# Performance work log

Measured on AMD Instinct MI355X. Metric: run time of the kernel, lower is better.

Reference implementation:

```python
import jax, jax.numpy as jnp
import numpy as np

N = 65536
H = 1024
E = 3  # experts: SwishGLU, GEGLU, ReGLU


def setup_inputs() -> dict:
    key = jax.random.key(0)
    ks = jax.random.split(key, 10)
    s = 1.0 / np.sqrt(H)
    return {
        "x": jax.random.normal(ks[0], (N, H), jnp.float32),
        "W1": jax.random.normal(ks[1], (E, H, H), jnp.float32) * s,
        "b1": jax.random.normal(ks[2], (E, H), jnp.float32) * s,
        "W2": jax.random.normal(ks[3], (E, H, H), jnp.float32) * s,
        "b2": jax.random.normal(ks[4], (E, H), jnp.float32) * s,
        "W3": jax.random.normal(ks[5], (E, H, H), jnp.float32) * s,
        "b3": jax.random.normal(ks[6], (E, H), jnp.float32) * s,
        "Wg": jax.random.normal(ks[7], (H, E), jnp.float32) * s,
        "bg": jax.random.normal(ks[8], (E,), jnp.float32) * s,
        "gumbel_u": jax.random.uniform(ks[9], (N, E), jnp.float32),
    }


def reference(x, W1, b1, W2, b2, W3, b3, Wg, bg, gumbel_u):
    # Gate: hard gumbel-softmax (tau=1, hard=True) with straight-through estimator
    logits = x @ Wg + bg                                   # [N, E]
    u = jnp.clip(gumbel_u, 1e-6, 1.0 - 1e-6)
    g = -jnp.log(-jnp.log(u))                              # Gumbel(0,1) noise
    y_soft = jax.nn.softmax(logits + g, axis=-1)           # [N, E]
    y_hard = jax.nn.one_hot(jnp.argmax(y_soft, axis=-1), E, dtype=x.dtype)
    gate = y_hard + y_soft - jax.lax.stop_gradient(y_soft)  # values == y_hard

    # Dense compute of all three GLU experts (faithful to original module)
    h1 = jnp.einsum('nd,edh->enh', x, W1) + b1[:, None, :]  # [E, N, H]
    h3 = jnp.einsum('nd,edh->enh', x, W3) + b3[:, None, :]  # [E, N, H]
    acts = jnp.stack([
        jax.nn.silu(h1[0]),                       # SwishGLU
        jax.nn.gelu(h1[1], approximate=False),    # GEGLU (exact erf gelu)
        jax.nn.relu(h1[2]),                       # ReGLU
    ], axis=0)                                    # [E, N, H]
    inner = acts * h3                             # [E, N, H]
    out_e = jnp.einsum('end,edh->enh', inner, W2) + b2[:, None, :]  # [E, N, H]

    # Select/mix with (hard) gate weights
    return jnp.einsum('enh,ne->nh', out_e, gate)  # [N, H]
```

## Files before the change

kernel.cpp:

```cpp
#include <hip/hip_runtime.h>
#include <math.h>

#define N_TOK 65536
#define H_DIM 1024

typedef __attribute__((ext_vector_type(8))) short bf16x8;
typedef __attribute__((ext_vector_type(4))) float f32x4;

static const size_t WS_CNT   = 0;
static const size_t WS_OFFS  = 64;
static const size_t WS_PERM  = 128;
static const size_t WS_WT13  = 1ull << 20;
static const size_t WS_WT2   = WS_WT13 + 12582912ull;
static const size_t WS_XB    = 20ull << 20;
static const size_t WS_INNER = WS_XB + 134217728ull;

static __device__ __forceinline__ unsigned short f2bf(float f) {
  union { float f; unsigned int u; } v; v.f = f;
  unsigned int r = v.u + 0x7fffu + ((v.u >> 16) & 1u);
  return (unsigned short)(r >> 16);
}

static __device__ __forceinline__ void gload16(const void* g, void* l) {
  __builtin_amdgcn_global_load_lds(
      (const __attribute__((address_space(1))) unsigned int*)g,
      (__attribute__((address_space(3))) unsigned int*)l, 16, 0, 0);
}

static __device__ __forceinline__ void bar() {
  asm volatile("" ::: "memory");
  __builtin_amdgcn_s_barrier();
  asm volatile("" ::: "memory");
}

__global__ void init_kernel(int* cnt) {
  if (threadIdx.x < 4) cnt[threadIdx.x] = 0;
}

__global__ __launch_bounds__(1024) void gate_kernel(
    const float* __restrict__ x, const float* __restrict__ Wg,
    const float* __restrict__ bg, const float* __restrict__ gu,
    unsigned short* __restrict__ xb, int* __restrict__ cnt,
    int* __restrict__ perm)
{
  __shared__ float wg[3072];
  __shared__ int bexp[16];
  for (int i = threadIdx.x; i < 3072; i += 1024) wg[i] = Wg[i];
  __syncthreads();
  const int wave = threadIdx.x >> 6;
  const int lane = threadIdx.x & 63;
  const int n0 = blockIdx.x * 16;
  const int n = n0 + wave;
  const float4* xrow = (const float4*)(x + (size_t)n * H_DIM);
  unsigned short* xbrow = xb + (size_t)n * H_DIM;
  float s0 = 0.f, s1 = 0.f, s2 = 0.f;
#pragma unroll
  for (int j = 0; j < 4; j++) {
    float4 v = xrow[j * 64 + lane];
    int d0 = (j * 64 + lane) * 4;
    const float* w = &wg[d0 * 3];
    s0 += v.x * w[0] + v.y * w[3] + v.z * w[6] + v.w * w[9];
    s1 += v.x * w[1] + v.y * w[4] + v.z * w[7] + v.w * w[10];
    s2 += v.x * w[2] + v.y * w[5] + v.z * w[8] + v.w * w[11];
    uint2 p;
    p.x = (unsigned)f2bf(v.x) | ((unsigned)f2bf(v.y) << 16);
    p.y = (unsigned)f2bf(v.z) | ((unsigned)f2bf(v.w) << 16);
    ((uint2*)xbrow)[j * 64 + lane] = p;
  }
#pragma unroll
  for (int o = 32; o; o >>= 1) {
    s0 += __shfl_xor(s0, o);
    s1 += __shfl_xor(s1, o);
    s2 += __shfl_xor(s2, o);
  }
  if (lane == 0) {
    const float* u = gu + (size_t)n * 3;
    float l[3] = { s0 + bg[0], s1 + bg[1], s2 + bg[2] };
    int best = 0; float bs = -1e30f;
#pragma unroll
    for (int e = 0; e < 3; e++) {
      float uc = fminf(fmaxf(u[e], 1e-6f), 1.f - 1e-6f);
      float g = -logf(-logf(uc));
      float s = l[e] + g;
      if (s > bs) { bs = s; best = e; }
    }
    bexp[wave] = best;
  }
  __syncthreads();
  if (threadIdx.x == 0) {
    int lc[3] = {0, 0, 0};
    int lpos[16];
    for (int w = 0; w < 16; w++) lpos[w] = lc[bexp[w]]++;
    int lbase[3];
    for (int e = 0; e < 3; e++)
      lbase[e] = lc[e] ? atomicAdd(&cnt[e], lc[e]) : 0;
    for (int w = 0; w < 16; w++) {
      int e = bexp[w];
      perm[e * N_TOK + lbase[e] + lpos[w]] = n0 + w;
    }
  }
}

__global__ void offs_kernel(const int* __restrict__ cnt, int* __restrict__ offs) {
  offs[0] = 0; offs[1] = cnt[0]; offs[2] = cnt[0] + cnt[1]; offs[3] = N_TOK;
}

__global__ __launch_bounds__(256) void wcvt_kernel(
    const float* __restrict__ W1, const float* __restrict__ W3,
    const float* __restrict__ W2,
    unsigned short* __restrict__ wt13, unsigned short* __restrict__ wt2)
{
  const int z = blockIdx.z, e = z / 3, m = z % 3;
  const float* src = (m == 0 ? W1 : (m == 1 ? W3 : W2)) + ((size_t)e << 20);
  __shared__ float t[32][33];
  const int h0 = blockIdx.x * 32, d0 = blockIdx.y * 32;
  const int tx = threadIdx.x, ty = threadIdx.y;
#pragma unroll
  for (int i = 0; i < 4; i++)
    t[ty + i * 8][tx] = src[(size_t)(d0 + ty + i * 8) * H_DIM + h0 + tx];
  __syncthreads();
#pragma unroll
  for (int i = 0; i < 4; i++) {
    const int h = h0 + ty + i * 8;
    const int kd = d0 + tx;
    const int kpos = (kd & ~63) | ((((kd >> 3) & 7) ^ (h & 7)) << 3) | (kd & 7);
    const unsigned short bv = f2bf(t[tx][ty + i * 8]);
    if (m == 2) {
      wt2[((size_t)e << 20) + ((size_t)h << 10) + kpos] = bv;
    } else {
      const int nc = ((h >> 4) << 5) + (m << 4) + (h & 15);
      wt13[((size_t)e << 21) + ((size_t)nc << 10) + kpos] = bv;
    }
  }
}

#define MFMA16(d, bb, aa) d = __builtin_amdgcn_mfma_f32_16x16x32_bf16((bb), (aa), (d), 0, 0, 0)

template<int PH>
__global__ __launch_bounds__(512, 2) void mlp_kernel(
    const unsigned short* __restrict__ A,
    const unsigned short* __restrict__ B,
    const float* __restrict__ bA, const float* __restrict__ bB,
    const int* __restrict__ cnt, const int* __restrict__ offs,
    const int* __restrict__ perm,
    unsigned short* __restrict__ inner, float* __restrict__ out)
{
  const int e = blockIdx.z;
  const int ce = cnt[e];
  const int m0 = blockIdx.y * 256;
  if (m0 >= ce) return;
  const int n0 = blockIdx.x * 256;
  const int oe = offs[e];

  __shared__ short smem[65536];

  const int tid = threadIdx.x;
  const int wid = tid >> 6, lane = tid & 63;
  const int wm = (wid >> 2) * 128, wn = (wid & 3) * 64;
  const int lr = lane & 15, quad = lane >> 4;
  const int xa = lane & 7;
  const int sl = lane >> 3, sc = lane & 7;

  unsigned aoff[4], boff[4];
  int ldsA[4], ldsB[4];
#pragma unroll
  for (int h = 0; h < 2; h++)
#pragma unroll
    for (int si = 0; si < 2; si++) {
      const int hs = h * 2 + si;
      const int rowb = h * 128 + (wid + si * 8) * 8;
      const int r = rowb + sl;
      unsigned arow;
      if constexpr (PH == 1) {
        arow = (unsigned)perm[e * N_TOK + min(m0 + r, ce - 1)];
      } else {
        arow = (unsigned)(oe + min(m0 + r, ce - 1));
      }
      aoff[hs] = (arow << 10) + (unsigned)((sc ^ sl) << 3);
      const unsigned brow = (PH == 1 ? ((unsigned)e << 11) : ((unsigned)e << 10))
                          + (unsigned)(n0 + r);
      boff[hs] = (brow << 10) + (unsigned)(sc << 3);
      ldsA[hs] = rowb * 64;
      ldsB[hs] = 16384 + rowb * 64;
    }

  f32x4 acc[8][4];
#pragma unroll
  for (int i = 0; i < 8; i++)
#pragma unroll
    for (int j = 0; j < 4; j++) acc[i][j] = (f32x4){0.f, 0.f, 0.f, 0.f};

#define ISSA(d, hs, k0) gload16(A + aoff[hs] + (k0), &smem[(d) * 32768 + ldsA[hs]])
#define ISSB(d, hs, k0) gload16(B + boff[hs] + (k0), &smem[(d) * 32768 + ldsB[hs]])
#define LDA_(mi, kx) (*(const bf16x8*)&As[(wm + (mi) * 16 + lr) * 64 + (((((kx) << 2) + quad) ^ xa) << 3)])
#define LDB_(nj, kx) (*(const bf16x8*)&Bs[(wn + (nj) * 16 + lr) * 64 + (((((kx) << 2) + quad) ^ xa) << 3)])

  ISSA(0, 0, 0);  ISSA(0, 1, 0);  ISSA(0, 2, 0);  ISSA(0, 3, 0);
  ISSB(0, 0, 0);  ISSB(0, 1, 0);  ISSB(0, 2, 0);  ISSB(0, 3, 0);
  ISSB(1, 0, 64); ISSB(1, 1, 64); ISSB(1, 2, 64); ISSB(1, 3, 64);
  asm volatile("s_waitcnt vmcnt(4)" ::: "memory");
  bar();

  for (int tt = 0; tt < 16; tt++) {
    const int cur = tt & 1, nxt = cur ^ 1;
    const short* As = smem + cur * 32768;
    const short* Bs = As + 16384;
    const int k1 = (tt + 1) << 6, k2 = (tt + 2) << 6;
    bf16x8 a0[4][2], a1[4][2], bfr[4][2];

#pragma unroll
    for (int mi = 0; mi < 4; mi++) { a0[mi][0] = LDA_(mi, 0); a0[mi][1] = LDA_(mi, 1); }
#pragma unroll
    for (int nj = 0; nj < 2; nj++) { bfr[nj][0] = LDB_(nj, 0); bfr[nj][1] = LDB_(nj, 1); }
    if (tt < 15) { ISSA(nxt, 0, k1); ISSA(nxt, 1, k1); }
    bar();
    __builtin_amdgcn_s_setprio(1);
#pragma unroll
    for (int mi = 0; mi < 4; mi++)
#pragma unroll
      for (int nj = 0; nj < 2; nj++) {
        MFMA16(acc[mi][nj], bfr[nj][0], a0[mi][0]);
        MFMA16(acc[mi][nj], bfr[nj][1], a0[mi][1]);
      }
    __builtin_amdgcn_s_setprio(0);
    bar();

#pragma unroll
    for (int nj = 2; nj < 4; nj++) { bfr[nj][0] = LDB_(nj, 0); bfr[nj][1] = LDB_(nj, 1); }
    if (tt < 15) { ISSA(nxt, 2, k1); ISSA(nxt, 3, k1); }
    bar();
    __builtin_amdgcn_s_setprio(1);
#pragma unroll
    for (int mi = 0; mi < 4; mi++)
#pragma unroll
      for (int nj = 2; nj < 4; nj++) {
        MFMA16(acc[mi][nj], bfr[nj][0], a0[mi][0]);
        MFMA16(acc[mi][nj], bfr[nj][1], a0[mi][1]);
      }
    __builtin_amdgcn_s_setprio(0);
    bar();

#pragma unroll
    for (int mi = 0; mi < 4; mi++) { a1[mi][0] = LDA_(mi + 4, 0); a1[mi][1] = LDA_(mi + 4, 1); }
    if (tt < 14) { ISSB(cur, 0, k2); ISSB(cur, 1, k2); }
    bar();
    __builtin_amdgcn_s_setprio(1);
#pragma unroll
    for (int mi = 0; mi < 4; mi++)
#pragma unroll
      for (int nj = 0; nj < 2; nj++) {
        MFMA16(acc[mi + 4][nj], bfr[nj][0], a1[mi][0]);
        MFMA16(acc[mi + 4][nj], bfr[nj][1], a1[mi][1]);
      }
    __builtin_amdgcn_s_setprio(0);
    bar();

    if (tt < 14) { ISSB(cur, 2, k2); ISSB(cur, 3, k2); }
    __builtin_amdgcn_s_setprio(1);
#pragma unroll
    for (int mi = 0; mi < 4; mi++)
#pragma unroll
      for (int nj = 2; nj < 4; nj++) {
        MFMA16(acc[mi + 4][nj], bfr[nj][0], a1[mi][0]);
        MFMA16(acc[mi + 4][nj], bfr[nj][1], a1[mi][1]);
      }
    __builtin_amdgcn_s_setprio(0);
    if (tt < 14)      asm volatile("s_waitcnt vmcnt(4)" ::: "memory");
    else if (tt < 15) asm volatile("s_waitcnt vmcnt(0)" ::: "memory");
    if (tt < 15) bar();
  }

#undef ISSA
#undef ISSB
#undef LDA_
#undef LDB_

  if constexpr (PH == 1) {
    const int colg = (((n0 + wn) >> 5) << 4) + quad * 4;
#pragma unroll
    for (int p = 0; p < 2; p++) {
      const int colb = colg + p * 16;
      const float4 v1 = *(const float4*)&bA[e * H_DIM + colb];
      const float4 v3 = *(const float4*)&bB[e * H_DIM + colb];
#pragma unroll
      for (int mi = 0; mi < 8; mi++) {
        const int rr = m0 + wm + mi * 16 + lr;
        if (rr < ce) {
          unsigned short sv[4];
#pragma unroll
          for (int r = 0; r < 4; r++) {
            const float h1 = acc[mi][2 * p][r]     + ((const float*)&v1)[r];
            const float h3 = acc[mi][2 * p + 1][r] + ((const float*)&v3)[r];
            float a;
            if (e == 0)      a = h1 / (1.f + expf(-h1));
            else if (e == 1) a = 0.5f * h1 * (1.f + erff(h1 * 0.70710678118f));
            else             a = fmaxf(h1, 0.f);
            sv[r] = f2bf(a * h3);
          }
          *(uint2*)&inner[((size_t)(oe + rr) << 10) + colb] = *(const uint2*)sv;
        }
      }
    }
  } else {
#pragma unroll
    for (int nj = 0; nj < 4; nj++) {
      const int colb = n0 + wn + nj * 16 + quad * 4;
      const float4 v2 = *(const float4*)&bA[e * H_DIM + colb];
#pragma unroll
      for (int mi = 0; mi < 8; mi++) {
        const int rr = m0 + wm + mi * 16 + lr;
        if (rr < ce) {
          const int g = perm[e * N_TOK + rr];
          float4 v;
          v.x = acc[mi][nj][0] + v2.x;
          v.y = acc[mi][nj][1] + v2.y;
          v.z = acc[mi][nj][2] + v2.z;
          v.w = acc[mi][nj][3] + v2.w;
          *(float4*)&out[((size_t)g << 10) + colb] = v;
        }
      }
    }
  }
}

extern "C" void kernel_launch(void* const* d_in, const int* in_sizes, int n_in,
                              void* d_out, int out_size, void* d_ws, size_t ws_size,
                              hipStream_t stream)
{
  const float* x  = (const float*)d_in[0];
  const float* W1 = (const float*)d_in[1];
  const float* b1 = (const float*)d_in[2];
  const float* W2 = (const float*)d_in[3];
  const float* b2 = (const float*)d_in[4];
  const float* W3 = (const float*)d_in[5];
  const float* b3 = (const float*)d_in[6];
  const float* Wg = (const float*)d_in[7];
  const float* bg = (const float*)d_in[8];
  const float* gu = (const float*)d_in[9];
  float* out = (float*)d_out;

  char* ws = (char*)d_ws;
  int* cnt  = (int*)(ws + WS_CNT);
  int* offs = (int*)(ws + WS_OFFS);
  int* perm = (int*)(ws + WS_PERM);
  unsigned short* wt13 = (unsigned short*)(ws + WS_WT13);
  unsigned short* wt2  = (unsigned short*)(ws + WS_WT2);
  unsigned short* xb   = (unsigned short*)(ws + WS_XB);
  unsigned short* inner = (unsigned short*)(ws + WS_INNER);

  init_kernel<<<1, 64, 0, stream>>>(cnt);
  gate_kernel<<<N_TOK / 16, 1024, 0, stream>>>(x, Wg, bg, gu, xb, cnt, perm);
  offs_kernel<<<1, 1, 0, stream>>>(cnt, offs);
  wcvt_kernel<<<dim3(32, 32, 9), dim3(32, 8), 0, stream>>>(W1, W3, W2, wt13, wt2);
  mlp_kernel<1><<<dim3(8, 256, 3), 512, 0, stream>>>(
      xb, wt13, b1, b3, cnt, offs, perm, inner, nullptr);
  mlp_kernel<2><<<dim3(4, 256, 3), 512, 0, stream>>>(
      inner, wt2, b2, nullptr, cnt, offs, perm, nullptr, out);
}
```

Baseline: 1.088 ms.

## Swizzle GEMM tile order, vectorize weight conversion, reorder MFMAs, fast SiLU

Several changes bundled together. The weight-transpose/convert kernel now uses 64-row tiles and writes 16-byte vector stores. The GEMM kernels remap the block index into groups of 8 M-tiles, intended to improve L2 reuse of the weight tiles. The MFMA loops are reordered so the two k-halves are interleaved across accumulators, and the main loop is unrolled by 2. SiLU now uses the hardware exp2 and reciprocal instructions, which are less precise than expf and a full division.

```diff
diff --git a/kernel.cpp b/kernel.cpp
--- a/kernel.cpp
+++ b/kernel.cpp
@@ -19,6 +19,13 @@
   union { float f; unsigned int u; } v; v.f = f;
   unsigned int r = v.u + 0x7fffu + ((v.u >> 16) & 1u);
   return (unsigned short)(r >> 16);
+}
+
+static __device__ __forceinline__ float fast_exp2(float x) {
+  float r; asm("v_exp_f32 %0, %1" : "=v"(r) : "v"(x)); return r;
+}
+static __device__ __forceinline__ float fast_rcp(float x) {
+  float r; asm("v_rcp_f32 %0, %1" : "=v"(r) : "v"(x)); return r;
 }
 
 static __device__ __forceinline__ void gload16(const void* g, void* l) {
@@ -112,25 +119,25 @@
 {
   const int z = blockIdx.z, e = z / 3, m = z % 3;
   const float* src = (m == 0 ? W1 : (m == 1 ? W3 : W2)) + ((size_t)e << 20);
-  __shared__ float t[32][33];
-  const int h0 = blockIdx.x * 32, d0 = blockIdx.y * 32;
-  const int tx = threadIdx.x, ty = threadIdx.y;
-#pragma unroll
-  for (int i = 0; i < 4; i++)
-    t[ty + i * 8][tx] = src[(size_t)(d0 + ty + i * 8) * H_DIM + h0 + tx];
+  __shared__ float t[64][33];
+  const int h0 = blockIdx.x * 32, d0 = blockIdx.y * 64;
+  const int tid = threadIdx.x;
+  const int lh = tid & 31, lk = tid >> 5;
+#pragma unroll
+  for (int j = 0; j < 8; j++)
+    t[j * 8 + lk][lh] = src[(size_t)(d0 + j * 8 + lk) * H_DIM + h0 + lh];
   __syncthreads();
-#pragma unroll
-  for (int i = 0; i < 4; i++) {
-    const int h = h0 + ty + i * 8;
-    const int kd = d0 + tx;
-    const int kpos = (kd & ~63) | ((((kd >> 3) & 7) ^ (h & 7)) << 3) | (kd & 7);
-    const unsigned short bv = f2bf(t[tx][ty + i * 8]);
-    if (m == 2) {
-      wt2[((size_t)e << 20) + ((size_t)h << 10) + kpos] = bv;
-    } else {
-      const int nc = ((h >> 4) << 5) + (m << 4) + (h & 15);
-      wt13[((size_t)e << 21) + ((size_t)nc << 10) + kpos] = bv;
-    }
+  const int h_l = tid >> 3, kc = tid & 7;
+  const int h = h0 + h_l;
+  unsigned short sv[8];
+#pragma unroll
+  for (int j = 0; j < 8; j++) sv[j] = f2bf(t[kc * 8 + j][h_l]);
+  const int kpos = d0 + ((kc ^ (h & 7)) << 3);
+  if (m == 2) {
+    *(uint4*)&wt2[((size_t)e << 20) + ((size_t)h << 10) + kpos] = *(const uint4*)sv;
+  } else {
+    const int nc = ((h >> 4) << 5) + (m << 4) + (h & 15);
+    *(uint4*)&wt13[((size_t)e << 21) + ((size_t)nc << 10) + kpos] = *(const uint4*)sv;
   }
 }
 
@@ -145,11 +152,15 @@
     const int* __restrict__ perm,
     unsigned short* __restrict__ inner, float* __restrict__ out)
 {
+  constexpr int NXT = (PH == 1) ? 8 : 4;
   const int e = blockIdx.z;
   const int ce = cnt[e];
-  const int m0 = blockIdx.y * 256;
+  const int f = blockIdx.x + NXT * blockIdx.y;
+  const int mt = (f & 7) + 8 * ((f >> 3) / NXT);
+  const int nt = (f >> 3) % NXT;
+  const int m0 = mt << 8;
   if (m0 >= ce) return;
-  const int n0 = blockIdx.x * 256;
+  const int n0 = nt << 8;
   const int oe = offs[e];
 
   __shared__ short smem[65536];
@@ -201,6 +212,7 @@
   asm volatile("s_waitcnt vmcnt(4)" ::: "memory");
   bar();
 
+#pragma unroll 2
   for (int tt = 0; tt < 16; tt++) {
     const int cur = tt & 1, nxt = cur ^ 1;
     const short* As = smem + cur * 32768;
@@ -216,12 +228,12 @@
     bar();
     __builtin_amdgcn_s_setprio(1);
 #pragma unroll
-    for (int mi = 0; mi < 4; mi++)
-#pragma unroll
-      for (int nj = 0; nj < 2; nj++) {
-        MFMA16(acc[mi][nj], bfr[nj][0], a0[mi][0]);
-        MFMA16(acc[mi][nj], bfr[nj][1], a0[mi][1]);
-      }
+    for (int kk = 0; kk < 2; kk++)
+#pragma unroll
+      for (int mi = 0; mi < 4; mi++)
+#pragma unroll
+        for (int nj = 0; nj < 2; nj++)
+          MFMA16(acc[mi][nj], bfr[nj][kk], a0[mi][kk]);
     __builtin_amdgcn_s_setprio(0);
     bar();
 
@@ -231,12 +243,12 @@
     bar();
     __builtin_amdgcn_s_setprio(1);
 #pragma unroll
-    for (int mi = 0; mi < 4; mi++)
-#pragma unroll
-      for (int nj = 2; nj < 4; nj++) {
-        MFMA16(acc[mi][nj], bfr[nj][0], a0[mi][0]);
-        MFMA16(acc[mi][nj], bfr[nj][1], a0[mi][1]);
-      }
+    for (int kk = 0; kk < 2; kk++)
+#pragma unroll
+      for (int mi = 0; mi < 4; mi++)
+#pragma unroll
+        for (int nj = 2; nj < 4; nj++)
+          MFMA16(acc[mi][nj], bfr[nj][kk], a0[mi][kk]);
     __builtin_amdgcn_s_setprio(0);
     bar();
 
@@ -246,24 +258,24 @@
     bar();
     __builtin_amdgcn_s_setprio(1);
 #pragma unroll
-    for (int mi = 0; mi < 4; mi++)
-#pragma unroll
-      for (int nj = 0; nj < 2; nj++) {
-        MFMA16(acc[mi + 4][nj], bfr[nj][0], a1[mi][0]);
-        MFMA16(acc[mi + 4][nj], bfr[nj][1], a1[mi][1]);
-      }
+    for (int kk = 0; kk < 2; kk++)
+#pragma unroll
+      for (int mi = 0; mi < 4; mi++)
+#pragma unroll
+        for (int nj = 0; nj < 2; nj++)
+          MFMA16(acc[mi + 4][nj], bfr[nj][kk], a1[mi][kk]);
     __builtin_amdgcn_s_setprio(0);
     bar();
 
     if (tt < 14) { ISSB(cur, 2, k2); ISSB(cur, 3, k2); }
     __builtin_amdgcn_s_setprio(1);
 #pragma unroll
-    for (int mi = 0; mi < 4; mi++)
-#pragma unroll
-      for (int nj = 2; nj < 4; nj++) {
-        MFMA16(acc[mi + 4][nj], bfr[nj][0], a1[mi][0]);
-        MFMA16(acc[mi + 4][nj], bfr[nj][1], a1[mi][1]);
-      }
+    for (int kk = 0; kk < 2; kk++)
+#pragma unroll
+      for (int mi = 0; mi < 4; mi++)
+#pragma unroll
+        for (int nj = 2; nj < 4; nj++)
+          MFMA16(acc[mi + 4][nj], bfr[nj][kk], a1[mi][kk]);
     __builtin_amdgcn_s_setprio(0);
     if (tt < 14)      asm volatile("s_waitcnt vmcnt(4)" ::: "memory");
     else if (tt < 15) asm volatile("s_waitcnt vmcnt(0)" ::: "memory");
@@ -292,7 +304,7 @@
             const float h1 = acc[mi][2 * p][r]     + ((const float*)&v1)[r];
             const float h3 = acc[mi][2 * p + 1][r] + ((const float*)&v3)[r];
             float a;
-            if (e == 0)      a = h1 / (1.f + expf(-h1));
+            if (e == 0)      a = h1 * fast_rcp(1.f + fast_exp2(h1 * -1.44269504f));
             else if (e == 1) a = 0.5f * h1 * (1.f + erff(h1 * 0.70710678118f));
             else             a = fmaxf(h1, 0.f);
             sv[r] = f2bf(a * h3);
@@ -351,7 +363,7 @@
   init_kernel<<<1, 64, 0, stream>>>(cnt);
   gate_kernel<<<N_TOK / 16, 1024, 0, stream>>>(x, Wg, bg, gu, xb, cnt, perm);
   offs_kernel<<<1, 1, 0, stream>>>(cnt, offs);
-  wcvt_kernel<<<dim3(32, 32, 9), dim3(32, 8), 0, stream>>>(W1, W3, W2, wt13, wt2);
+  wcvt_kernel<<<dim3(32, 16, 9), 256, 0, stream>>>(W1, W3, W2, wt13, wt2);
   mlp_kernel<1><<<dim3(8, 256, 3), 512, 0, stream>>>(
       xb, wt13, b1, b3, cnt, offs, perm, inner, nullptr);
   mlp_kernel<2><<<dim3(4, 256, 3), 512, 0, stream>>>(
```

New measurement: 1.056 ms. 2.9% less time.
